# Kernel tuning notes

Measured on AMD Instinct MI355X. Metric: run time of the kernel, lower is better.

## Reference

```python
import jax, jax.numpy as jnp
import numpy as np

TEMPERATURE = 2.0
RAD2DEG = 180.0 / np.pi


def _safe_norm(diff, axis=-1):
    # L2 norm with zero (sub)gradient at 0, matching torch's convention and
    # avoiding NaNs on the (later-discarded) diagonal of pairwise distances.
    d2 = jnp.sum(diff * diff, axis=axis)
    pos = d2 > 0
    return jnp.where(pos, jnp.sqrt(jnp.where(pos, d2, 1.0)), 0.0)


def _rot6d_to_matrix(d6):
    # pytorch3d.transforms.rotation_6d_to_matrix: Gram-Schmidt on two 3-vectors.
    a1, a2 = d6[..., :3], d6[..., 3:6]
    b1 = a1 / jnp.linalg.norm(a1, axis=-1, keepdims=True)
    a2p = a2 - jnp.sum(b1 * a2, axis=-1, keepdims=True) * b1
    b2 = a2p / jnp.linalg.norm(a2p, axis=-1, keepdims=True)
    b3 = jnp.cross(b1, b2)
    return jnp.stack([b1, b2, b3], axis=-2)  # [n, 3, 3], rows b1,b2,b3


def _pose_error(pose):
    rot = _rot6d_to_matrix(pose[:, :6])                    # [n,3,3]
    div = jnp.power(jnp.linalg.det(rot), 1.0 / 3.0)[:, None, None]
    rot = rot / div
    t = pose[:, 6:]                                        # [n,3]
    # trace(rot_i @ rot_j^T) = sum_ab rot_i[a,b]*rot_j[a,b]
    r_trace = jnp.einsum('iab,jab->ij', rot, rot)          # [n,n]
    cos_theta = (r_trace - 1.0) / 2.0
    theta = jnp.arccos(jnp.clip(cos_theta, -1.0, 1.0)) * RAD2DEG
    shift = _safe_norm(t[:, None, :] - t[None, :, :]) * 100.0
    return theta, shift


def reference(features, labels):
    n = features.shape[0]
    theta_diffs, shift_diffs = _pose_error(labels)

    # FeatureSimilarity('l2'): -||f_i - f_j|| / t
    logits = -_safe_norm(features[:, None, :] - features[None, :, :]) / TEMPERATURE
    logits = logits - jax.lax.stop_gradient(jnp.max(logits, axis=1, keepdims=True))
    exp_logits = jnp.exp(logits)

    # Drop diagonal -> [n, n-1], preserving ascending column order (masked_select).
    cols = jnp.arange(n - 1)
    jidx = cols[None, :] + (cols[None, :] >= jnp.arange(n)[:, None]).astype(cols.dtype)
    take = lambda x: jnp.take_along_axis(x, jidx, axis=1)
    L = take(logits)          # [n, n-1]
    E = take(exp_logits)      # [n, n-1]
    TD = take(theta_diffs)    # [n, n-1]
    SD = take(shift_diffs)    # [n, n-1]

    # Vectorize the k-loop: M[i,k,j] = diffs[i,j] >= diffs[i,k]
    mt = TD[:, None, :] >= TD[:, :, None]                 # [n, n-1, n-1]
    ms = SD[:, None, :] >= SD[:, :, None]
    denom_t = jnp.sum(jnp.where(mt, E[:, None, :], 0.0), axis=-1)  # [n, n-1]
    denom_s = jnp.sum(jnp.where(ms, E[:, None, :], 0.0), axis=-1)

    pos_log_probs = (2.0 * L - jnp.log(denom_t) - jnp.log(denom_s)) / 2.0
    return -jnp.sum(pos_log_probs) / (n * (n - 1))


def setup_inputs() -> dict:
    key = jax.random.key(0)
    k1, k2 = jax.random.split(key)
    features = jax.random.normal(k1, (512, 256), dtype=jnp.float32)
    labels = jax.random.normal(k2, (512, 9), dtype=jnp.float32)
    return {"features": features, "labels": labels}
```

## Files before the change

kernel.cpp:

```cpp
#include <hip/hip_runtime.h>
#include <math.h>

#define N 512
#define D 256
#define NPAIRS 261632.0f

typedef unsigned long long u64;
#define SW(x) ((x) ^ (((x) >> 4) & 15))

__constant__ float kRad2Deg = 57.29577951308232f;

__global__ __launch_bounds__(64) void prep_kernel(
        const float* __restrict__ f,
        const float* __restrict__ labels,
        float* __restrict__ rot,
        float* __restrict__ tvec,
        float* __restrict__ nrm,
        float* __restrict__ acc,
        unsigned* __restrict__ cnt) {
    const int i = blockIdx.x;
    const int l = threadIdx.x;

    const float4 v = ((const float4*)(f + i * D))[l];
    float ss = v.x * v.x + v.y * v.y + v.z * v.z + v.w * v.w;
#pragma unroll
    for (int off = 32; off > 0; off >>= 1) ss += __shfl_down(ss, off, 64);

    if (l == 0) {
        nrm[i] = ss;
        const float* p = labels + i * 9;
        float a1x = p[0], a1y = p[1], a1z = p[2];
        float a2x = p[3], a2y = p[4], a2z = p[5];
        float n1 = sqrtf(a1x * a1x + a1y * a1y + a1z * a1z);
        float b1x = a1x / n1, b1y = a1y / n1, b1z = a1z / n1;
        float dp = b1x * a2x + b1y * a2y + b1z * a2z;
        float cx = a2x - dp * b1x, cy = a2y - dp * b1y, cz = a2z - dp * b1z;
        float n2 = sqrtf(cx * cx + cy * cy + cz * cz);
        float b2x = cx / n2, b2y = cy / n2, b2z = cz / n2;
        float b3x = b1y * b2z - b1z * b2y;
        float b3y = b1z * b2x - b1x * b2z;
        float b3z = b1x * b2y - b1y * b2x;
        float det = b1x * (b2y * b3z - b2z * b3y)
                  - b1y * (b2x * b3z - b2z * b3x)
                  + b1z * (b2x * b3y - b2y * b3x);
        float inv = 1.0f / cbrtf(det);
        float* r = rot + i * 9;
        r[0] = b1x * inv; r[1] = b1y * inv; r[2] = b1z * inv;
        r[3] = b2x * inv; r[4] = b2y * inv; r[5] = b2z * inv;
        r[6] = b3x * inv; r[7] = b3y * inv; r[8] = b3z * inv;
        tvec[i * 3 + 0] = p[6];
        tvec[i * 3 + 1] = p[7];
        tvec[i * 3 + 2] = p[8];
        if (i == 0) { acc[0] = 0.0f; cnt[0] = 0u; }
    }
}

__global__ __launch_bounds__(512) void fused_row_kernel(
        const float* __restrict__ f,
        const float* __restrict__ rot,
        const float* __restrict__ tvec,
        const float* __restrict__ nrm,
        float* __restrict__ acc,
        unsigned* __restrict__ cnt,
        float* __restrict__ out) {
    __shared__ __attribute__((aligned(16))) float4 lds_fi[D / 4];
    __shared__ u64   qT[512], qS[512];
    __shared__ float sT[512], sS[512];
    __shared__ int   lT[512], lS[512];
    __shared__ float redA[8], redB[8], redC[8];
    __shared__ float sh_dT, sh_dS;

    const int t  = threadIdx.x;
    const int i  = blockIdx.x;
    const int tp = t & 255;
    const int lane = t & 63, wid = t >> 6;

    if (t < D / 4) lds_fi[t] = ((const float4*)(f + i * D))[t];
    __syncthreads();

    float dot = 0.0f;
    const float4* __restrict__ fj4 = (const float4*)(f + t * D);
#pragma unroll 8
    for (int kk = 0; kk < D / 4; ++kk) {
        const float4 v = fj4[kk];
        const float4 a = lds_fi[kk];
        dot += a.x * v.x; dot += a.y * v.y; dot += a.z * v.z; dot += a.w * v.w;
    }

    float rj[9];
#pragma unroll
    for (int c = 0; c < 9; ++c) rj[c] = rot[t * 9 + c];
    float tr = 0.0f;
#pragma unroll
    for (int c = 0; c < 9; ++c) tr += rot[i * 9 + c] * rj[c];
    float ct = (tr - 1.0f) * 0.5f;
    ct = fminf(1.0f, fmaxf(-1.0f, ct));
    const float theta = acosf(ct) * kRad2Deg;

    const float dx = tvec[i * 3 + 0] - tvec[t * 3 + 0];
    const float dy = tvec[i * 3 + 1] - tvec[t * 3 + 1];
    const float dz = tvec[i * 3 + 2] - tvec[t * 3 + 2];
    const float sd2 = dx * dx + dy * dy + dz * dz;
    const float shift = (sd2 > 0.0f ? sqrtf(sd2) : 0.0f) * 100.0f;

    const float d2 = nrm[i] + nrm[t] - 2.0f * dot;
    float L, Ev;
    if (t == i) { L = 0.0f; Ev = 0.0f; }
    else {
        const float dist = (d2 > 0.0f ? sqrtf(d2) : 0.0f);
        L  = -dist * 0.5f;
        Ev = expf(L);
    }

    if (t == i) { sh_dT = theta; sh_dS = shift; }
    const u64 eb = (u64)__float_as_uint(Ev);
    qT[SW(t)] = ((u64)__float_as_uint(theta) << 32) | eb;
    qS[SW(t)] = ((u64)__float_as_uint(shift) << 32) | eb;
    __syncthreads();

    float dtd = (theta >= sh_dT) ? Ev : 0.0f;
    float dsd = (shift >= sh_dS) ? Ev : 0.0f;
    float lpart = L;
#pragma unroll
    for (int off = 32; off > 0; off >>= 1) {
        dtd   += __shfl_down(dtd, off, 64);
        dsd   += __shfl_down(dsd, off, 64);
        lpart += __shfl_down(lpart, off, 64);
    }
    if (lane == 0) { redA[wid] = dtd; redB[wid] = dsd; redC[wid] = lpart; }

    for (unsigned k = 2; k <= 512; k <<= 1) {
        for (unsigned jj = k >> 1; jj >= 1; jj >>= 1) {
            __syncthreads();
            const unsigned a = ((tp & ~(jj - 1)) << 1) | (tp & (jj - 1));
            const unsigned b = a | jj;
            const bool up = ((a & k) == 0);
            if (t < 256) {
                u64 va = qT[SW(a)], vb = qT[SW(b)];
                if (up ? (va > vb) : (va < vb)) { qT[SW(a)] = vb; qT[SW(b)] = va; }
            } else {
                u64 va = qS[SW(a)], vb = qS[SW(b)];
                if (up ? (va > vb) : (va < vb)) { qS[SW(a)] = vb; qS[SW(b)] = va; }
            }
        }
    }
    __syncthreads();

    float diag_part = 0.0f, lsum = 0.0f;
    if (t == 0) {
        float a = 0.0f, b = 0.0f;
#pragma unroll
        for (int w = 0; w < 8; ++w) { a += redA[w]; b += redB[w]; lsum += redC[w]; }
        diag_part = 0.5f * (logf(a) + logf(b));
    }

    if (t < 256) {
        const u64 v0 = qT[SW(tp)], v1 = qT[SW(tp + 256)];
        sT[tp]       = __uint_as_float((unsigned)v0);
        sT[tp + 256] = __uint_as_float((unsigned)v1);
        const unsigned h0 = (unsigned)(v0 >> 32), h1 = (unsigned)(v1 >> 32);
        const unsigned hp = (unsigned)(qT[SW(tp + 255)] >> 32);
        lT[tp]       = (tp == 0 || (unsigned)(qT[SW(tp - 1)] >> 32) != h0) ? tp : 0;
        lT[tp + 256] = (hp != h1) ? (tp + 256) : 0;
    } else {
        const u64 v0 = qS[SW(tp)], v1 = qS[SW(tp + 256)];
        sS[tp]       = __uint_as_float((unsigned)v0);
        sS[tp + 256] = __uint_as_float((unsigned)v1);
        const unsigned h0 = (unsigned)(v0 >> 32), h1 = (unsigned)(v1 >> 32);
        const unsigned hp = (unsigned)(qS[SW(tp + 255)] >> 32);
        lS[tp]       = (tp == 0 || (unsigned)(qS[SW(tp - 1)] >> 32) != h0) ? tp : 0;
        lS[tp + 256] = (hp != h1) ? (tp + 256) : 0;
    }
    __syncthreads();

    for (int st = 1; st < 512; st <<= 1) {
        float a0, a1; int m0, m1;
        if (t < 256) {
            a0 = (tp + st < 512) ? sT[tp + st] : 0.0f;
            a1 = (tp + 256 + st < 512) ? sT[tp + 256 + st] : 0.0f;
            m0 = (tp >= st) ? lT[tp - st] : 0;
            m1 = lT[tp + 256 - st];
        } else {
            a0 = (tp + st < 512) ? sS[tp + st] : 0.0f;
            a1 = (tp + 256 + st < 512) ? sS[tp + 256 + st] : 0.0f;
            m0 = (tp >= st) ? lS[tp - st] : 0;
            m1 = lS[tp + 256 - st];
        }
        __syncthreads();
        if (t < 256) {
            sT[tp] += a0; sT[tp + 256] += a1;
            lT[tp] = max(lT[tp], m0); lT[tp + 256] = max(lT[tp + 256], m1);
        } else {
            sS[tp] += a0; sS[tp + 256] += a1;
            lS[tp] = max(lS[tp], m0); lS[tp + 256] = max(lS[tp + 256], m1);
        }
        __syncthreads();
    }

    float term = logf(sT[lT[t]]) + logf(sS[lS[t]]);
#pragma unroll
    for (int off = 32; off > 0; off >>= 1) term += __shfl_down(term, off, 64);
    __syncthreads();
    if (lane == 0) redA[wid] = term;
    __syncthreads();

    if (t == 0) {
        float tt = 0.0f;
#pragma unroll
        for (int w = 0; w < 8; ++w) tt += redA[w];
        atomicAdd(acc, lsum - 0.5f * tt + diag_part);
        __threadfence();
        const unsigned old = atomicAdd(cnt, 1u);
        if (old == (unsigned)(gridDim.x - 1)) {
            const float total = atomicAdd(acc, 0.0f);
            out[0] = -total / NPAIRS;
        }
    }
}

extern "C" void kernel_launch(void* const* d_in, const int* in_sizes, int n_in,
                              void* d_out, int out_size, void* d_ws, size_t ws_size,
                              hipStream_t stream) {
    const float* f      = (const float*)d_in[0];
    const float* labels = (const float*)d_in[1];
    float* out = (float*)d_out;
    float* ws  = (float*)d_ws;

    float*    rot  = ws;
    float*    tvec = rot + N * 9;
    float*    nrm  = tvec + N * 3;
    float*    acc  = nrm + N;
    unsigned* cnt  = (unsigned*)(acc + 1);

    prep_kernel<<<N, 64, 0, stream>>>(f, labels, rot, tvec, nrm, acc, cnt);
    fused_row_kernel<<<N, 512, 0, stream>>>(f, rot, tvec, nrm, acc, cnt, out);
}
```

Before: 60.44 us.

## Split into tiled Gram kernel and wave-level register bitonic sort row kernel

Computes the feature Gram matrix with a separate LDS-tiled 16x16 kernel instead of each row block re-reading all features from global memory. The row kernel now assigns one wave per (row, key) pair and does the bitonic sort, suffix sum and segment-head propagation entirely in registers with cross-lane shuffles, removing LDS traffic and block-wide barriers. This adds a third kernel launch and a round trip of the 512x512 Gram matrix through global memory.

```diff
diff --git a/kernel.cpp b/kernel.cpp
--- a/kernel.cpp
+++ b/kernel.cpp
@@ -6,9 +6,16 @@
 #define NPAIRS 261632.0f
 
 typedef unsigned long long u64;
-#define SW(x) ((x) ^ (((x) >> 4) & 15))
+typedef unsigned int u32;
 
 __constant__ float kRad2Deg = 57.29577951308232f;
+
+__device__ __forceinline__ u64 shfl_xor_u64(u64 v, int m) {
+    u32 lo = (u32)v, hi = (u32)(v >> 32);
+    lo = (u32)__shfl_xor((int)lo, m, 64);
+    hi = (u32)__shfl_xor((int)hi, m, 64);
+    return ((u64)hi << 32) | (u64)lo;
+}
 
 __global__ __launch_bounds__(64) void prep_kernel(
         const float* __restrict__ f,
@@ -55,163 +62,210 @@
     }
 }
 
-__global__ __launch_bounds__(512) void fused_row_kernel(
+__global__ __launch_bounds__(256) void gram_kernel(
         const float* __restrict__ f,
+        float* __restrict__ G) {
+    __shared__ __attribute__((aligned(16))) float As[16][68];
+    __shared__ __attribute__((aligned(16))) float Bs[16][68];
+    const int tx = threadIdx.x & 15, ty = threadIdx.x >> 4;
+    const int bi = (blockIdx.x >> 5) << 4;
+    const int bj = (blockIdx.x & 31) << 4;
+
+    float accv = 0.0f;
+#pragma unroll
+    for (int k0 = 0; k0 < D; k0 += 64) {
+        const float4 av = *(const float4*)(f + (bi + ty) * D + k0 + tx * 4);
+        const float4 bv = *(const float4*)(f + (bj + ty) * D + k0 + tx * 4);
+        __syncthreads();
+        *(float4*)&As[ty][tx * 4] = av;
+        *(float4*)&Bs[ty][tx * 4] = bv;
+        __syncthreads();
+#pragma unroll
+        for (int kk = 0; kk < 16; ++kk) {
+            const float4 a = *(const float4*)&As[ty][kk * 4];
+            const float4 b = *(const float4*)&Bs[tx][kk * 4];
+            accv += a.x * b.x; accv += a.y * b.y;
+            accv += a.z * b.z; accv += a.w * b.w;
+        }
+    }
+    G[(bi + ty) * N + bj + tx] = accv;
+}
+
+__global__ __launch_bounds__(256) void row_kernel(
+        const float* __restrict__ G,
         const float* __restrict__ rot,
         const float* __restrict__ tvec,
         const float* __restrict__ nrm,
         float* __restrict__ acc,
         unsigned* __restrict__ cnt,
         float* __restrict__ out) {
-    __shared__ __attribute__((aligned(16))) float4 lds_fi[D / 4];
-    __shared__ u64   qT[512], qS[512];
-    __shared__ float sT[512], sS[512];
-    __shared__ int   lT[512], lS[512];
-    __shared__ float redA[8], redB[8], redC[8];
-    __shared__ float sh_dT, sh_dS;
-
-    const int t  = threadIdx.x;
-    const int i  = blockIdx.x;
-    const int tp = t & 255;
-    const int lane = t & 63, wid = t >> 6;
-
-    if (t < D / 4) lds_fi[t] = ((const float4*)(f + i * D))[t];
-    __syncthreads();
-
-    float dot = 0.0f;
-    const float4* __restrict__ fj4 = (const float4*)(f + t * D);
-#pragma unroll 8
-    for (int kk = 0; kk < D / 4; ++kk) {
-        const float4 v = fj4[kk];
-        const float4 a = lds_fi[kk];
-        dot += a.x * v.x; dot += a.y * v.y; dot += a.z * v.z; dot += a.w * v.w;
-    }
-
-    float rj[9];
-#pragma unroll
-    for (int c = 0; c < 9; ++c) rj[c] = rot[t * 9 + c];
-    float tr = 0.0f;
-#pragma unroll
-    for (int c = 0; c < 9; ++c) tr += rot[i * 9 + c] * rj[c];
-    float ct = (tr - 1.0f) * 0.5f;
-    ct = fminf(1.0f, fmaxf(-1.0f, ct));
-    const float theta = acosf(ct) * kRad2Deg;
-
-    const float dx = tvec[i * 3 + 0] - tvec[t * 3 + 0];
-    const float dy = tvec[i * 3 + 1] - tvec[t * 3 + 1];
-    const float dz = tvec[i * 3 + 2] - tvec[t * 3 + 2];
-    const float sd2 = dx * dx + dy * dy + dz * dz;
-    const float shift = (sd2 > 0.0f ? sqrtf(sd2) : 0.0f) * 100.0f;
-
-    const float d2 = nrm[i] + nrm[t] - 2.0f * dot;
-    float L, Ev;
-    if (t == i) { L = 0.0f; Ev = 0.0f; }
-    else {
-        const float dist = (d2 > 0.0f ? sqrtf(d2) : 0.0f);
-        L  = -dist * 0.5f;
-        Ev = expf(L);
-    }
-
-    if (t == i) { sh_dT = theta; sh_dS = shift; }
-    const u64 eb = (u64)__float_as_uint(Ev);
-    qT[SW(t)] = ((u64)__float_as_uint(theta) << 32) | eb;
-    qS[SW(t)] = ((u64)__float_as_uint(shift) << 32) | eb;
-    __syncthreads();
-
-    float dtd = (theta >= sh_dT) ? Ev : 0.0f;
-    float dsd = (shift >= sh_dS) ? Ev : 0.0f;
-    float lpart = L;
+    const int tid  = threadIdx.x;
+    const int lane = tid & 63;
+    const int wid  = tid >> 6;
+    const int i    = blockIdx.x * 2 + (wid >> 1);
+    const bool isT = (wid & 1) == 0;
+
+    float rotI[9];
+#pragma unroll
+    for (int c = 0; c < 9; ++c) rotI[c] = rot[i * 9 + c];
+    const float tIx = tvec[i * 3 + 0];
+    const float tIy = tvec[i * 3 + 1];
+    const float tIz = tvec[i * 3 + 2];
+    const float ni  = nrm[i];
+
+    float dthr;
+    if (isT) {
+        float trii = 0.0f;
+#pragma unroll
+        for (int c = 0; c < 9; ++c) trii += rotI[c] * rotI[c];
+        float ctv = fminf(1.0f, fmaxf(-1.0f, (trii - 1.0f) * 0.5f));
+        dthr = acosf(ctv) * kRad2Deg;
+    } else {
+        dthr = 0.0f;
+    }
+
+    u64 q[8];
+    float lsum = 0.0f, dden = 0.0f;
+#pragma unroll
+    for (int r = 0; r < 8; ++r) {
+        const int e = r * 64 + lane;
+        const float gij = G[i * N + e];
+        const float d2  = ni + nrm[e] - 2.0f * gij;
+        float L, Ev;
+        if (e == i) { L = 0.0f; Ev = 0.0f; }
+        else {
+            const float dist = (d2 > 0.0f) ? sqrtf(d2) : 0.0f;
+            L  = -0.5f * dist;
+            Ev = expf(L);
+        }
+        float keyv;
+        if (isT) {
+            float tr8 = 0.0f;
+#pragma unroll
+            for (int c = 0; c < 9; ++c) tr8 += rotI[c] * rot[e * 9 + c];
+            float ctv = fminf(1.0f, fmaxf(-1.0f, (tr8 - 1.0f) * 0.5f));
+            keyv = acosf(ctv) * kRad2Deg;
+        } else {
+            const float dx = tIx - tvec[e * 3 + 0];
+            const float dy = tIy - tvec[e * 3 + 1];
+            const float dz = tIz - tvec[e * 3 + 2];
+            const float sd2 = dx * dx + dy * dy + dz * dz;
+            keyv = ((sd2 > 0.0f) ? sqrtf(sd2) : 0.0f) * 100.0f;
+        }
+        q[r]  = ((u64)__float_as_uint(keyv) << 32) | (u64)__float_as_uint(Ev);
+        lsum += L;
+        dden += (keyv >= dthr) ? Ev : 0.0f;
+    }
 #pragma unroll
     for (int off = 32; off > 0; off >>= 1) {
-        dtd   += __shfl_down(dtd, off, 64);
-        dsd   += __shfl_down(dsd, off, 64);
-        lpart += __shfl_down(lpart, off, 64);
-    }
-    if (lane == 0) { redA[wid] = dtd; redB[wid] = dsd; redC[wid] = lpart; }
-
-    for (unsigned k = 2; k <= 512; k <<= 1) {
-        for (unsigned jj = k >> 1; jj >= 1; jj >>= 1) {
-            __syncthreads();
-            const unsigned a = ((tp & ~(jj - 1)) << 1) | (tp & (jj - 1));
-            const unsigned b = a | jj;
-            const bool up = ((a & k) == 0);
-            if (t < 256) {
-                u64 va = qT[SW(a)], vb = qT[SW(b)];
-                if (up ? (va > vb) : (va < vb)) { qT[SW(a)] = vb; qT[SW(b)] = va; }
+        lsum += __shfl_down(lsum, off, 64);
+        dden += __shfl_down(dden, off, 64);
+    }
+
+#pragma unroll
+    for (int kb = 1; kb <= 9; ++kb) {
+        const unsigned k = 1u << kb;
+#pragma unroll
+        for (int jb = kb - 1; jb >= 0; --jb) {
+            if (jb >= 6) {
+                const int rx = 1 << (jb - 6);
+#pragma unroll
+                for (int r = 0; r < 8; ++r) {
+                    if ((r & rx) == 0) {
+                        const int rp = r | rx;
+                        const bool up = ((((unsigned)r << 6) & k) == 0);
+                        const u64 a = q[r], b = q[rp];
+                        const bool altb = a < b;
+                        const u64 mn = altb ? a : b;
+                        const u64 mx = altb ? b : a;
+                        q[r]  = up ? mn : mx;
+                        q[rp] = up ? mx : mn;
+                    }
+                }
             } else {
-                u64 va = qS[SW(a)], vb = qS[SW(b)];
-                if (up ? (va > vb) : (va < vb)) { qS[SW(a)] = vb; qS[SW(b)] = va; }
+                const int jj = 1 << jb;
+#pragma unroll
+                for (int r = 0; r < 8; ++r) {
+                    const u64 p = shfl_xor_u64(q[r], jj);
+                    bool up;
+                    if (kb >= 6) up = ((((unsigned)r << 6) & k) == 0);
+                    else         up = ((lane & k) == 0);
+                    const bool lower   = ((lane & jj) == 0);
+                    const bool keepmin = (up == lower);
+                    const u64 a = q[r];
+                    const bool altb = a < p;
+                    q[r] = (altb == keepmin) ? a : p;
+                }
             }
         }
     }
-    __syncthreads();
-
-    float diag_part = 0.0f, lsum = 0.0f;
-    if (t == 0) {
-        float a = 0.0f, b = 0.0f;
-#pragma unroll
-        for (int w = 0; w < 8; ++w) { a += redA[w]; b += redB[w]; lsum += redC[w]; }
-        diag_part = 0.5f * (logf(a) + logf(b));
-    }
-
-    if (t < 256) {
-        const u64 v0 = qT[SW(tp)], v1 = qT[SW(tp + 256)];
-        sT[tp]       = __uint_as_float((unsigned)v0);
-        sT[tp + 256] = __uint_as_float((unsigned)v1);
-        const unsigned h0 = (unsigned)(v0 >> 32), h1 = (unsigned)(v1 >> 32);
-        const unsigned hp = (unsigned)(qT[SW(tp + 255)] >> 32);
-        lT[tp]       = (tp == 0 || (unsigned)(qT[SW(tp - 1)] >> 32) != h0) ? tp : 0;
-        lT[tp + 256] = (hp != h1) ? (tp + 256) : 0;
-    } else {
-        const u64 v0 = qS[SW(tp)], v1 = qS[SW(tp + 256)];
-        sS[tp]       = __uint_as_float((unsigned)v0);
-        sS[tp + 256] = __uint_as_float((unsigned)v1);
-        const unsigned h0 = (unsigned)(v0 >> 32), h1 = (unsigned)(v1 >> 32);
-        const unsigned hp = (unsigned)(qS[SW(tp + 255)] >> 32);
-        lS[tp]       = (tp == 0 || (unsigned)(qS[SW(tp - 1)] >> 32) != h0) ? tp : 0;
-        lS[tp + 256] = (hp != h1) ? (tp + 256) : 0;
-    }
-    __syncthreads();
-
-    for (int st = 1; st < 512; st <<= 1) {
-        float a0, a1; int m0, m1;
-        if (t < 256) {
-            a0 = (tp + st < 512) ? sT[tp + st] : 0.0f;
-            a1 = (tp + 256 + st < 512) ? sT[tp + 256 + st] : 0.0f;
-            m0 = (tp >= st) ? lT[tp - st] : 0;
-            m1 = lT[tp + 256 - st];
-        } else {
-            a0 = (tp + st < 512) ? sS[tp + st] : 0.0f;
-            a1 = (tp + 256 + st < 512) ? sS[tp + 256 + st] : 0.0f;
-            m0 = (tp >= st) ? lS[tp - st] : 0;
-            m1 = lS[tp + 256 - st];
-        }
-        __syncthreads();
-        if (t < 256) {
-            sT[tp] += a0; sT[tp + 256] += a1;
-            lT[tp] = max(lT[tp], m0); lT[tp + 256] = max(lT[tp + 256], m1);
-        } else {
-            sS[tp] += a0; sS[tp + 256] += a1;
-            lS[tp] = max(lS[tp], m0); lS[tp + 256] = max(lS[tp + 256], m1);
-        }
-        __syncthreads();
-    }
-
-    float term = logf(sT[lT[t]]) + logf(sS[lS[t]]);
-#pragma unroll
-    for (int off = 32; off > 0; off >>= 1) term += __shfl_down(term, off, 64);
-    __syncthreads();
-    if (lane == 0) redA[wid] = term;
-    __syncthreads();
-
-    if (t == 0) {
-        float tt = 0.0f;
-#pragma unroll
-        for (int w = 0; w < 8; ++w) tt += redA[w];
-        atomicAdd(acc, lsum - 0.5f * tt + diag_part);
+
+    u32 key[8]; float sfx[8];
+#pragma unroll
+    for (int r = 0; r < 8; ++r) {
+        key[r] = (u32)(q[r] >> 32);
+        sfx[r] = __uint_as_float((u32)q[r]);
+    }
+
+#pragma unroll
+    for (int off = 1; off < 64; off <<= 1) {
+#pragma unroll
+        for (int r = 0; r < 8; ++r) {
+            const float t = __shfl_down(sfx[r], off, 64);
+            if (lane + off < 64) sfx[r] += t;
+        }
+    }
+    {
+        float carry = 0.0f;
+#pragma unroll
+        for (int r = 7; r >= 0; --r) {
+            const float tot = __shfl(sfx[r], 0, 64);
+            sfx[r] += carry;
+            carry  += tot;
+        }
+    }
+
+    float hv[8];
+#pragma unroll
+    for (int r = 0; r < 8; ++r) {
+        u32 kprev = (u32)__shfl_up((int)key[r], 1, 64);
+        if (r > 0) {
+            const u32 c = (u32)__shfl((int)key[r - 1], 63, 64);
+            kprev = (lane == 0) ? c : kprev;
+        }
+        const bool head = (r == 0 && lane == 0) ? true : (key[r] != kprev);
+        hv[r] = head ? sfx[r] : -1.0f;
+    }
+#pragma unroll
+    for (int off = 1; off < 64; off <<= 1) {
+#pragma unroll
+        for (int r = 0; r < 8; ++r) {
+            const float t = __shfl_up(hv[r], off, 64);
+            if (lane >= off && hv[r] < 0.0f) hv[r] = t;
+        }
+    }
+    {
+        float carry2 = 0.0f;
+#pragma unroll
+        for (int r = 0; r < 8; ++r) {
+            if (hv[r] < 0.0f) hv[r] = carry2;
+            carry2 = __shfl(hv[r], 63, 64);
+        }
+    }
+
+    float tsum = 0.0f;
+#pragma unroll
+    for (int r = 0; r < 8; ++r) tsum += logf(hv[r]);
+#pragma unroll
+    for (int off = 32; off > 0; off >>= 1) tsum += __shfl_down(tsum, off, 64);
+
+    if (lane == 0) {
+        float contrib = -0.5f * tsum + 0.5f * logf(dden);
+        if (isT) contrib += lsum;
+        atomicAdd(acc, contrib);
         __threadfence();
         const unsigned old = atomicAdd(cnt, 1u);
-        if (old == (unsigned)(gridDim.x - 1)) {
+        if (old == (unsigned)(gridDim.x * 4 - 1)) {
             const float total = atomicAdd(acc, 0.0f);
             out[0] = -total / NPAIRS;
         }
@@ -231,7 +285,9 @@
     float*    nrm  = tvec + N * 3;
     float*    acc  = nrm + N;
     unsigned* cnt  = (unsigned*)(acc + 1);
+    float*    G    = acc + 16;
 
     prep_kernel<<<N, 64, 0, stream>>>(f, labels, rot, tvec, nrm, acc, cnt);
-    fused_row_kernel<<<N, 512, 0, stream>>>(f, rot, tvec, nrm, acc, cnt, out);
-}
+    gram_kernel<<<(N / 16) * (N / 16), 256, 0, stream>>>(f, G);
+    row_kernel<<<N / 2, 256, 0, stream>>>(G, rot, tvec, nrm, acc, cnt, out);
+}
```

New measurement: 58.87 us. 1.03x faster.
